# Kernel tuning notes

Measured on AMD Instinct MI355X. Metric: run time of the kernel, lower is better.

The kernel has to match this reference:

```python
import jax, jax.numpy as jnp
import numpy as np

B = 1024
NIF = 2048   # n_image_features
V = 10000    # vocab_size
E = 512      # embedding_dim
H = 1024     # hidden_size
L = 32       # max_sentence_length
ND = 3       # num distractors


def _lstm_cell(x, h, c, Wih, Whh, bih, bhh):
    # torch LSTMCell: gates ordered i, f, g, o
    g = x @ Wih.T + bih + h @ Whh.T + bhh
    i, f, gc, o = jnp.split(g, 4, axis=-1)
    c = jax.nn.sigmoid(f) * c + jax.nn.sigmoid(i) * jnp.tanh(gc)
    h = jax.nn.sigmoid(o) * jnp.tanh(c)
    return h, c


def setup_inputs() -> dict:
    key = jax.random.key(0)
    ks = jax.random.split(key, 20)
    s = 0.02
    inp = {
        "target": jax.random.normal(ks[0], (B, NIF), jnp.float32),
        "distractors": jax.random.normal(ks[1], (ND, B, NIF), jnp.float32),
        "start_token_idx": 1,
        "max_sentence_length": L,
        # Sender params
        "W_aff": s * jax.random.normal(ks[2], (H, NIF), jnp.float32),
        "b_aff": jnp.zeros((H,), jnp.float32),
        "emb_s": s * jax.random.normal(ks[3], (V, E), jnp.float32),
        "Wih_s": s * jax.random.normal(ks[4], (4 * H, E), jnp.float32),
        "Whh_s": s * jax.random.normal(ks[5], (4 * H, H), jnp.float32),
        "bih_s": jnp.zeros((4 * H,), jnp.float32),
        "bhh_s": jnp.zeros((4 * H,), jnp.float32),
        "Wp": s * jax.random.normal(ks[6], (V, H), jnp.float32),
        "bp": jnp.zeros((V,), jnp.float32),
        # Receiver params
        "emb_r": s * jax.random.normal(ks[7], (V, E), jnp.float32),
        "Wih_r": s * jax.random.normal(ks[8], (4 * H, E), jnp.float32),
        "Whh_r": s * jax.random.normal(ks[9], (4 * H, H), jnp.float32),
        "bih_r": jnp.zeros((4 * H,), jnp.float32),
        "bhh_r": jnp.zeros((4 * H,), jnp.float32),
        "W_out": s * jax.random.normal(ks[10], (NIF, H), jnp.float32),
        "b_out": jnp.zeros((NIF,), jnp.float32),
    }
    return inp


def reference(target, distractors, start_token_idx, max_sentence_length,
              W_aff, b_aff, emb_s, Wih_s, Whh_s, bih_s, bhh_s, Wp, bp,
              emb_r, Wih_r, Whh_r, bih_r, bhh_r, W_out, b_out):
    Bt = target.shape[0]

    # ---- Sender: greedy decode (eval-mode argmax, matching greedy=True) ----
    h0 = target @ W_aff.T + b_aff
    c0 = jnp.zeros_like(h0)
    w0 = emb_s[jnp.full((Bt,), start_token_idx, dtype=jnp.int32)]

    def send_step(carry, _):
        h, c, w = carry
        h, c = _lstm_cell(w, h, c, Wih_s, Whh_s, bih_s, bhh_s)
        logits = h @ Wp.T + bp                         # [B, V]
        idx = jnp.argmax(logits, axis=-1)              # greedy token
        logp = jnp.take_along_axis(jax.nn.log_softmax(logits, axis=-1),
                                   idx[:, None], axis=-1)[:, 0]
        w = emb_s[idx]
        return (h, c, w), (idx, logp)

    _, (message, logps) = jax.lax.scan(send_step, (h0, c0, w0), None,
                                       length=max_sentence_length)
    message = message.T            # [B, L]
    log_prob = logps[-1]           # log_prob of last sampled word, [B]

    # ---- Receiver: encode message ----
    hr = jnp.zeros((Bt, H), jnp.float32)
    cr = jnp.zeros((Bt, H), jnp.float32)

    def recv_step(carry, w_idx):
        h, c = carry
        h, c = _lstm_cell(emb_r[w_idx], h, c, Wih_r, Whh_r, bih_r, bhh_r)
        return (h, c), None

    (hr, cr), _ = jax.lax.scan(recv_step, (hr, cr), message.T)
    r = hr @ W_out.T + b_out       # [B, NIF]

    # ---- Hinge loss over distractors ----
    r_T = r.T                                       # [NIF, B]
    t_r = target @ r_T                              # [B, B]
    d_r = jnp.einsum('nbf,fc->nbc', distractors, r_T)  # [ND, B, B]
    loss = jnp.sum(jnp.maximum(0.0, 1.0 - t_r[None] + d_r), axis=0)  # [B, B]
    loss = -loss * log_prob        # broadcast [B] over last dim, as in torch
    return jnp.mean(loss)
```

## Files before the change

kernel.cpp:

```cpp
#include <hip/hip_runtime.h>
#include <hip/hip_bf16.h>
#include <cstdint>
#include <cstddef>

#define Bc   1024
#define NIFc 2048
#define Vc   10000
#define Ec   512
#define Hc   1024
#define Lc   32
#define NDc  3
#define G4c  4096
#define NTv  79
#define TMLD 80

typedef __attribute__((ext_vector_type(4))) float f32x4;
typedef __attribute__((ext_vector_type(8))) short s16x8;
typedef __attribute__((ext_vector_type(4))) short s16x4;

#define GBM 128
#define GBN 128
#define GBK 64

__device__ __forceinline__ void gld_lds16(void* lds, const void* g) {
    __builtin_amdgcn_global_load_lds(
        (const __attribute__((address_space(1))) unsigned int*)g,
        (__attribute__((address_space(3))) unsigned int*)lds,
        16, 0, 0);
}

__device__ __forceinline__ void gemm_body(
    const __hip_bfloat16* __restrict__ A, int lda,
    const __hip_bfloat16* __restrict__ W, int ldw,
    const float* __restrict__ bias, float* __restrict__ C,
    int M, int N, int K, int bx, int by,
    float* __restrict__ tile_max, int tmld)
{
    __shared__ __align__(16) __hip_bfloat16 As[GBM * GBK];
    __shared__ __align__(16) __hip_bfloat16 Ws[GBN * GBK];
    __shared__ float smax[GBM];

    const int tid  = threadIdx.x;
    const int lane = tid & 63;
    const int wave = tid >> 6;
    const int m0 = by * GBM;
    const int n0 = bx * GBN;

    const __hip_bfloat16* ag[4];
    const __hip_bfloat16* wg[4];
    #pragma unroll
    for (int r = 0; r < 4; ++r) {
        int p = r * 256 + tid;
        int m = p >> 3;
        int q = (p & 7) ^ (m & 7);
        ag[r] = A + (size_t)(m0 + m) * lda + q * 8;
        int wn = n0 + m; if (wn >= N) wn = N - 1;
        wg[r] = W + (size_t)wn * ldw + q * 8;
    }

    f32x4 acc[4][4];
    #pragma unroll
    for (int i = 0; i < 4; ++i)
        #pragma unroll
        for (int j = 0; j < 4; ++j)
            acc[i][j] = (f32x4)(0.0f);

    const int hm = (wave & 1) << 6;
    const int hn = (wave >> 1) << 6;
    const int lm = lane & 15;
    const int quad = lane >> 4;

    const int nk = K >> 6;
    for (int kt = 0; kt < nk; ++kt) {
        __syncthreads();
        #pragma unroll
        for (int r = 0; r < 4; ++r) {
            int ldsbase = (r * 256 + wave * 64) * 8;
            gld_lds16(As + ldsbase, ag[r]);
            gld_lds16(Ws + ldsbase, wg[r]);
            ag[r] += GBK;
            wg[r] += GBK;
        }
        __syncthreads();
        #pragma unroll
        for (int c = 0; c < 2; ++c) {
            s16x8 af[4], wf[4];
            int q = c * 4 + quad;
            #pragma unroll
            for (int i = 0; i < 4; ++i) {
                int m = hm + i * 16 + lm;
                af[i] = *(const s16x8*)(As + ((m << 3) + (q ^ (m & 7))) * 8);
                int n = hn + i * 16 + lm;
                wf[i] = *(const s16x8*)(Ws + ((n << 3) + (q ^ (n & 7))) * 8);
            }
            #pragma unroll
            for (int i = 0; i < 4; ++i)
                #pragma unroll
                for (int j = 0; j < 4; ++j)
                    acc[i][j] = __builtin_amdgcn_mfma_f32_16x16x32_bf16(
                        af[i], wf[j], acc[i][j], 0, 0, 0);
        }
    }

    float rowmax[4][4];
    #pragma unroll
    for (int i = 0; i < 4; ++i)
        #pragma unroll
        for (int rr = 0; rr < 4; ++rr)
            rowmax[i][rr] = -__builtin_inff();

    #pragma unroll
    for (int i = 0; i < 4; ++i) {
        int mbase = m0 + hm + i * 16 + quad * 4;
        #pragma unroll
        for (int j = 0; j < 4; ++j) {
            int n = n0 + hn + j * 16 + lm;
            if (n < N) {
                float bv = bias ? bias[n] : 0.0f;
                #pragma unroll
                for (int rr = 0; rr < 4; ++rr) {
                    float v = acc[i][j][rr] + bv;
                    C[(size_t)(mbase + rr) * N + n] = v;
                    rowmax[i][rr] = fmaxf(rowmax[i][rr], v);
                }
            }
        }
    }

    if (tile_max) {
        #pragma unroll
        for (int i = 0; i < 4; ++i)
            #pragma unroll
            for (int rr = 0; rr < 4; ++rr) {
                float v = rowmax[i][rr];
                v = fmaxf(v, __shfl_xor(v, 1));
                v = fmaxf(v, __shfl_xor(v, 2));
                v = fmaxf(v, __shfl_xor(v, 4));
                v = fmaxf(v, __shfl_xor(v, 8));
                rowmax[i][rr] = v;
            }
        __syncthreads();
        if (hn == 0 && lm == 0) {
            #pragma unroll
            for (int i = 0; i < 4; ++i)
                #pragma unroll
                for (int rr = 0; rr < 4; ++rr)
                    smax[hm + i * 16 + quad * 4 + rr] = rowmax[i][rr];
        }
        __syncthreads();
        if (hn == 64 && lm == 0) {
            #pragma unroll
            for (int i = 0; i < 4; ++i)
                #pragma unroll
                for (int rr = 0; rr < 4; ++rr) {
                    int r = hm + i * 16 + quad * 4 + rr;
                    smax[r] = fmaxf(smax[r], rowmax[i][rr]);
                }
        }
        __syncthreads();
        if (tid < GBM)
            tile_max[(size_t)(m0 + tid) * tmld + bx] = smax[tid];
    }
}

__global__ __launch_bounds__(256) void gemm_bf16_tn(
    const __hip_bfloat16* __restrict__ A, int lda,
    const __hip_bfloat16* __restrict__ W, int ldw,
    const float* __restrict__ bias, float* __restrict__ C,
    int M, int N, int K, float* __restrict__ tile_max, int tmld)
{
    gemm_body(A, lda, W, ldw, bias, C, M, N, K, blockIdx.x, blockIdx.y,
              tile_max, tmld);
}

__global__ __launch_bounds__(256) void gemm_bf16_sk2(
    const __hip_bfloat16* __restrict__ A, int lda,
    const __hip_bfloat16* __restrict__ W, int ldw,
    float* __restrict__ Cpart, int M, int N, int Ksub)
{
    int z = blockIdx.z;
    gemm_body(A + (size_t)z * Ksub, lda, W + (size_t)z * Ksub, ldw, nullptr,
              Cpart + (size_t)z * M * N, M, N, Ksub, blockIdx.x, blockIdx.y,
              nullptr, 0);
}

__global__ __launch_bounds__(256) void split3_a_kernel(
    const float* __restrict__ in, int ldin,
    __hip_bfloat16* __restrict__ out, int ldo, int coff, int M, int K)
{
    int i = blockIdx.x * 256 + threadIdx.x;
    if (i >= M * K) return;
    int m = i / K, k = i - m * K;
    float v = in[(size_t)m * ldin + k];
    __hip_bfloat16 hi = __float2bfloat16(v);
    float lo = v - __bfloat162float(hi);
    __hip_bfloat16* row = out + (size_t)m * ldo + coff;
    row[k] = hi;
    row[K + k] = __float2bfloat16(lo);
    row[2 * K + k] = hi;
}

__global__ __launch_bounds__(256) void split3_w_kernel(
    const float* __restrict__ in, int ldin,
    __hip_bfloat16* __restrict__ out, int ldo, int coff, int M, int K)
{
    int i = blockIdx.x * 256 + threadIdx.x;
    if (i >= M * K) return;
    int m = i / K, k = i - m * K;
    float v = in[(size_t)m * ldin + k];
    __hip_bfloat16 hi = __float2bfloat16(v);
    float lo = v - __bfloat162float(hi);
    __hip_bfloat16* row = out + (size_t)m * ldo + coff;
    row[k] = hi;
    row[K + k] = hi;
    row[2 * K + k] = __float2bfloat16(lo);
}

__global__ __launch_bounds__(256) void cast2d_kernel(
    const float* __restrict__ in, int ldin,
    __hip_bfloat16* __restrict__ out, int ldo, int coff, int M, int K)
{
    int i = blockIdx.x * 256 + threadIdx.x;
    if (i >= M * K) return;
    int m = i / K, k = i - m * K;
    out[(size_t)m * ldo + coff + k] = __float2bfloat16(in[(size_t)m * ldin + k]);
}

__global__ __launch_bounds__(256) void gather_split3_kernel(
    const float* __restrict__ emb, int E, const int* __restrict__ idx,
    int stride, __hip_bfloat16* __restrict__ out, int ldo, int Brows)
{
    int i = blockIdx.x * 256 + threadIdx.x;
    if (i >= Brows * E) return;
    int b = i / E, k = i - b * E;
    float v = emb[(size_t)idx[b * stride] * E + k];
    __hip_bfloat16 hi = __float2bfloat16(v);
    float lo = v - __bfloat162float(hi);
    __hip_bfloat16* row = out + (size_t)b * ldo;
    row[k] = hi;
    row[E + k] = __float2bfloat16(lo);
    row[2 * E + k] = hi;
}

__global__ __launch_bounds__(256) void gather_cast_kernel(
    const float* __restrict__ emb, int E, const int* __restrict__ idx,
    __hip_bfloat16* __restrict__ out, int ldo, int coff, int Brows)
{
    int i = blockIdx.x * 256 + threadIdx.x;
    if (i >= Brows * E) return;
    int b = i / E, k = i - b * E;
    out[(size_t)b * ldo + coff + k] =
        __float2bfloat16(emb[(size_t)idx[b] * E + k]);
}

__global__ __launch_bounds__(256) void add_vec_kernel(
    const float* __restrict__ a, const float* __restrict__ b,
    float* __restrict__ o, int n)
{
    int i = blockIdx.x * 256 + threadIdx.x;
    if (i < n) o[i] = a[i] + b[i];
}

__device__ __forceinline__ short bf16bits(float x) {
    __hip_bfloat16 t = __float2bfloat16(x);
    return *reinterpret_cast<short*>(&t);
}

__global__ __launch_bounds__(256) void lstm_fused_s(
    const float* __restrict__ gp0, const float* __restrict__ gp1,
    const float* __restrict__ bias, float* __restrict__ h,
    float* __restrict__ c, __hip_bfloat16* __restrict__ xh3)
{
    int i = blockIdx.x * 256 + threadIdx.x;
    if (i >= Bc * Hc / 4) return;
    int b = i >> 8;
    int j = (i & 255) * 4;
    size_t g0 = (size_t)b * G4c + j;
    f32x4 gi = *(const f32x4*)(gp0 + g0) + *(const f32x4*)(gp1 + g0)
             + *(const f32x4*)(bias + j);
    f32x4 gf = *(const f32x4*)(gp0 + g0 + Hc) + *(const f32x4*)(gp1 + g0 + Hc)
             + *(const f32x4*)(bias + Hc + j);
    f32x4 gg = *(const f32x4*)(gp0 + g0 + 2 * Hc) + *(const f32x4*)(gp1 + g0 + 2 * Hc)
             + *(const f32x4*)(bias + 2 * Hc + j);
    f32x4 go = *(const f32x4*)(gp0 + g0 + 3 * Hc) + *(const f32x4*)(gp1 + g0 + 3 * Hc)
             + *(const f32x4*)(bias + 3 * Hc + j);
    size_t hix = (size_t)b * Hc + j;
    f32x4 cv = *(const f32x4*)(c + hix);
    f32x4 cn, hv;
    s16x4 hi4, lo4;
    #pragma unroll
    for (int k = 0; k < 4; ++k) {
        float si = 1.0f / (1.0f + expf(-gi[k]));
        float sf = 1.0f / (1.0f + expf(-gf[k]));
        float so = 1.0f / (1.0f + expf(-go[k]));
        float cc = sf * cv[k] + si * tanhf(gg[k]);
        cn[k] = cc;
        float hh = so * tanhf(cc);
        hv[k] = hh;
        hi4[k] = bf16bits(hh);
        lo4[k] = bf16bits(hh - __bfloat162float(__float2bfloat16(hh)));
    }
    *(f32x4*)(c + hix) = cn;
    *(f32x4*)(h + hix) = hv;
    __hip_bfloat16* row = xh3 + (size_t)b * 4608 + 1536;
    *(s16x4*)(row + j) = hi4;
    *(s16x4*)(row + Hc + j) = lo4;
    *(s16x4*)(row + 2 * Hc + j) = hi4;
}

__global__ __launch_bounds__(256) void combine_h0_kernel(
    const float* __restrict__ p0, const float* __restrict__ p1,
    const float* __restrict__ bias, float* __restrict__ h,
    __hip_bfloat16* __restrict__ xh3)
{
    int i = blockIdx.x * 256 + threadIdx.x;
    if (i >= Bc * Hc / 4) return;
    int b = i >> 8;
    int j = (i & 255) * 4;
    size_t ix = (size_t)b * Hc + j;
    f32x4 v = *(const f32x4*)(p0 + ix) + *(const f32x4*)(p1 + ix)
            + *(const f32x4*)(bias + j);
    *(f32x4*)(h + ix) = v;
    s16x4 hi4, lo4;
    #pragma unroll
    for (int k = 0; k < 4; ++k) {
        hi4[k] = bf16bits(v[k]);
        lo4[k] = bf16bits(v[k] - __bfloat162float(__float2bfloat16(v[k])));
    }
    __hip_bfloat16* row = xh3 + (size_t)b * 4608 + 1536;
    *(s16x4*)(row + j) = hi4;
    *(s16x4*)(row + Hc + j) = lo4;
    *(s16x4*)(row + 2 * Hc + j) = hi4;
}

__global__ __launch_bounds__(256) void lstm_fused_r(
    const float* __restrict__ gp0, const float* __restrict__ gp1,
    const float* __restrict__ bias, float* __restrict__ h,
    float* __restrict__ c, __hip_bfloat16* __restrict__ xh_r,
    const float* __restrict__ emb, const int* __restrict__ msg_next)
{
    int i = blockIdx.x * 256 + threadIdx.x;
    if (i >= Bc * Hc / 4) return;
    int b = i >> 8;
    int j = (i & 255) * 4;
    size_t g0 = (size_t)b * G4c + j;
    f32x4 gi = *(const f32x4*)(gp0 + g0) + *(const f32x4*)(gp1 + g0)
             + *(const f32x4*)(bias + j);
    f32x4 gf = *(const f32x4*)(gp0 + g0 + Hc) + *(const f32x4*)(gp1 + g0 + Hc)
             + *(const f32x4*)(bias + Hc + j);
    f32x4 gg = *(const f32x4*)(gp0 + g0 + 2 * Hc) + *(const f32x4*)(gp1 + g0 + 2 * Hc)
             + *(const f32x4*)(bias + 2 * Hc + j);
    f32x4 go = *(const f32x4*)(gp0 + g0 + 3 * Hc) + *(const f32x4*)(gp1 + g0 + 3 * Hc)
             + *(const f32x4*)(bias + 3 * Hc + j);
    size_t hix = (size_t)b * Hc + j;
    f32x4 cv = *(const f32x4*)(c + hix);
    f32x4 cn, hv;
    s16x4 hb4;
    #pragma unroll
    for (int k = 0; k < 4; ++k) {
        float si = 1.0f / (1.0f + expf(-gi[k]));
        float sf = 1.0f / (1.0f + expf(-gf[k]));
        float so = 1.0f / (1.0f + expf(-go[k]));
        float cc = sf * cv[k] + si * tanhf(gg[k]);
        cn[k] = cc;
        float hh = so * tanhf(cc);
        hv[k] = hh;
        hb4[k] = bf16bits(hh);
    }
    *(f32x4*)(c + hix) = cn;
    *(f32x4*)(h + hix) = hv;
    *(s16x4*)(xh_r + (size_t)b * 1536 + Ec + j) = hb4;
    if (msg_next && j < Ec) {
        int tok = msg_next[b];
        f32x4 e = *(const f32x4*)(emb + (size_t)tok * Ec + j);
        s16x4 eb;
        #pragma unroll
        for (int k = 0; k < 4; ++k) eb[k] = bf16bits(e[k]);
        *(s16x4*)(xh_r + (size_t)b * 1536 + j) = eb;
    }
}

__global__ __launch_bounds__(256) void argmax_rescore_v3(
    const float* __restrict__ logits, const float* __restrict__ tmax,
    const float* __restrict__ h, const float* __restrict__ Wp,
    const float* __restrict__ bp, const float* __restrict__ emb,
    int* __restrict__ msg_t, float* __restrict__ logp,
    __hip_bfloat16* __restrict__ xh3, int want_logp)
{
    const int b = blockIdx.x;
    const int tid = threadIdx.x;
    const int lane = tid & 63;
    const int wave = tid >> 6;
    const float* row = logits + (size_t)b * Vc;

    __shared__ float stm[128];
    __shared__ float redm[256];
    __shared__ float reds[256];
    __shared__ int   qt[32];
    __shared__ int   nq, cnt;
    __shared__ int   cand[64];
    __shared__ float score[64];
    __shared__ float sbestv;
    __shared__ int   sbestj;

    float tv = (tid < NTv) ? tmax[(size_t)b * TMLD + tid] : -__builtin_inff();
    if (tid < 128) stm[tid] = tv;
    redm[tid] = tv;
    reds[tid] = (tid < NTv) ? tv : 0.0f;
    if (tid == 0) { nq = 0; cnt = 0; }
    __syncthreads();
    #pragma unroll
    for (int s = 128; s > 0; s >>= 1) {
        if (tid < s) {
            redm[tid] = fmaxf(redm[tid], redm[tid + s]);
            reds[tid] += reds[tid + s];
        }
        __syncthreads();
    }
    const float m = redm[0];
    const float spread = m - reds[0] * (1.0f / NTv);
    const float delta = 0.08f * spread + 1e-6f * (1.0f + fabsf(m));

    if (tid < NTv && stm[tid] >= m - delta) {
        int k = atomicAdd(&nq, 1);
        if (k < 32) qt[k] = tid;
    }
    __syncthreads();
    int nqt = nq < 32 ? nq : 32;

    for (int qi = 0; qi < nqt; qi += 2) {
        int ti = qi + (tid >> 7);
        if (ti < nqt) {
            int j = qt[ti] * 128 + (tid & 127);
            if (j < Vc) {
                float v = row[j];
                if (v >= m - delta) {
                    int k = atomicAdd(&cnt, 1);
                    if (k < 64) cand[k] = j;
                }
            }
        }
    }
    __syncthreads();
    int nc = cnt < 64 ? cnt : 64;

    const float* hrow = h + (size_t)b * Hc;
    for (int cix = wave; cix < nc; cix += 4) {
        int j = cand[cix];
        const float* wrow = Wp + (size_t)j * Hc;
        float part = 0.0f;
        #pragma unroll
        for (int kk = 0; kk < 4; ++kk) {
            int k = kk * 256 + lane * 4;
            f32x4 hv = *(const f32x4*)(hrow + k);
            f32x4 wv = *(const f32x4*)(wrow + k);
            part = fmaf(hv.x, wv.x, part);
            part = fmaf(hv.y, wv.y, part);
            part = fmaf(hv.z, wv.z, part);
            part = fmaf(hv.w, wv.w, part);
        }
        #pragma unroll
        for (int off = 1; off < 64; off <<= 1)
            part += __shfl_xor(part, off);
        if (lane == 0) score[cix] = part + bp[j];
    }
    __syncthreads();
    if (tid == 0) {
        float bv = -__builtin_inff();
        int bj = 0x7fffffff;
        for (int cix = 0; cix < nc; ++cix) {
            float v = score[cix];
            int j = cand[cix];
            if (v > bv || (v == bv && j < bj)) { bv = v; bj = j; }
        }
        sbestv = bv;
        sbestj = bj;
        msg_t[b] = bj;
    }
    __syncthreads();
    const int bestj = sbestj;

    if (want_logp) {
        float s = 0.0f;
        const f32x4* row4 = (const f32x4*)row;
        for (int j = tid; j < Vc / 4; j += 256) {
            f32x4 v = row4[j];
            s += expf(v.x - m) + expf(v.y - m) + expf(v.z - m) + expf(v.w - m);
        }
        redm[tid] = s;
        __syncthreads();
        #pragma unroll
        for (int st = 128; st > 0; st >>= 1) {
            if (tid < st) redm[tid] += redm[tid + st];
            __syncthreads();
        }
        if (tid == 0) logp[b] = sbestv - (m + logf(redm[0]));
    }

    if (xh3 && tid < 128) {
        int k = tid * 4;
        f32x4 e = *(const f32x4*)(emb + (size_t)bestj * Ec + k);
        s16x4 hi4, lo4;
        #pragma unroll
        for (int kk = 0; kk < 4; ++kk) {
            hi4[kk] = bf16bits(e[kk]);
            lo4[kk] = bf16bits(e[kk] - __bfloat162float(__float2bfloat16(e[kk])));
        }
        __hip_bfloat16* orow = xh3 + (size_t)b * 4608;
        *(s16x4*)(orow + k) = hi4;
        *(s16x4*)(orow + Ec + k) = lo4;
        *(s16x4*)(orow + 2 * Ec + k) = hi4;
    }
}

__global__ __launch_bounds__(256) void hinge_kernel(
    const float* __restrict__ S, const float* __restrict__ logp,
    float* __restrict__ partials, int Bn)
{
    int tid = threadIdx.x;
    int n = Bn * Bn;
    float acc = 0.0f;
    for (int idx = blockIdx.x * 256 + tid; idx < n; idx += gridDim.x * 256) {
        int j = idx & (Bn - 1);
        float s0 = S[idx];
        float l = fmaxf(0.0f, 1.0f - s0 + S[n + idx])
                + fmaxf(0.0f, 1.0f - s0 + S[2 * n + idx])
                + fmaxf(0.0f, 1.0f - s0 + S[3 * n + idx]);
        acc += l * logp[j];
    }
    __shared__ float sv[256];
    sv[tid] = acc;
    __syncthreads();
    for (int s = 128; s > 0; s >>= 1) {
        if (tid < s) sv[tid] += sv[tid + s];
        __syncthreads();
    }
    if (tid == 0) partials[blockIdx.x] = sv[0];
}

__global__ __launch_bounds__(256) void final_reduce_kernel(
    const float* __restrict__ partials, int np, float* __restrict__ out,
    float scale)
{
    int tid = threadIdx.x;
    float acc = 0.0f;
    for (int i = tid; i < np; i += 256) acc += partials[i];
    __shared__ float sv[256];
    sv[tid] = acc;
    __syncthreads();
    for (int s = 128; s > 0; s >>= 1) {
        if (tid < s) sv[tid] += sv[tid + s];
        __syncthreads();
    }
    if (tid == 0) out[0] = sv[0] * scale;
}

extern "C" void kernel_launch(void* const* d_in, const int* in_sizes, int n_in,
                              void* d_out, int out_size, void* d_ws, size_t ws_size,
                              hipStream_t stream)
{
    (void)in_sizes; (void)n_in; (void)out_size; (void)ws_size;

    const float* target  = (const float*)d_in[0];
    const float* distr   = (const float*)d_in[1];
    const int*   start_t = (const int*)d_in[2];
    const float* W_aff = (const float*)d_in[4];
    const float* b_aff = (const float*)d_in[5];
    const float* emb_s = (const float*)d_in[6];
    const float* Wih_s = (const float*)d_in[7];
    const float* Whh_s = (const float*)d_in[8];
    const float* bih_s = (const float*)d_in[9];
    const float* bhh_s = (const float*)d_in[10];
    const float* Wp    = (const float*)d_in[11];
    const float* bp    = (const float*)d_in[12];
    const float* emb_r = (const float*)d_in[13];
    const float* Wih_r = (const float*)d_in[14];
    const float* Whh_r = (const float*)d_in[15];
    const float* bih_r = (const float*)d_in[16];
    const float* bhh_r = (const float*)d_in[17];
    const float* W_out = (const float*)d_in[18];
    const float* b_out = (const float*)d_in[19];

    dim3 blk(256);

    char* b0 = (char*)d_ws;
    size_t off = 0;
    auto take = [&](size_t bytes) -> char* {
        char* p = b0 + off;
        off += (bytes + 511) & ~(size_t)511;
        return p;
    };
    const size_t MB = 1024 * 1024;
    __hip_bfloat16* WihWhh3 = (__hip_bfloat16*)take((size_t)G4c * 4608 * 2);
    __hip_bfloat16* Wp_b    = (__hip_bfloat16*)take((size_t)Vc * Hc * 2);
    __hip_bfloat16* WihWhh_r= (__hip_bfloat16*)take((size_t)G4c * 1536 * 2);
    __hip_bfloat16* W_out_b = (__hip_bfloat16*)take((size_t)NIFc * Hc * 2);
    __hip_bfloat16* xh3     = (__hip_bfloat16*)take((size_t)Bc * 4608 * 2);
    __hip_bfloat16* xh_r    = (__hip_bfloat16*)take((size_t)Bc * 1536 * 2);
    float* gates_p = (float*)take((size_t)2 * Bc * G4c * 4);
    float* h_s    = (float*)take((size_t)Bc * Hc * 4);
    float* c_s    = (float*)take((size_t)Bc * Hc * 4);
    float* hr     = (float*)take((size_t)Bc * Hc * 4);
    float* cr     = (float*)take((size_t)Bc * Hc * 4);
    float* logp   = (float*)take(Bc * 4);
    int*   msg    = (int*)take((size_t)Lc * Bc * 4);
    float* parts  = (float*)take(1024 * 4);
    float* bias_s = (float*)take(G4c * 4);
    float* bias_r = (float*)take(G4c * 4);
    float* tilemax= (float*)take((size_t)Bc * TMLD * 4);
    char*  U      = take(48 * MB);

    __hip_bfloat16* target3 = (__hip_bfloat16*)U;
    __hip_bfloat16* W_aff3  = (__hip_bfloat16*)(U + 13 * MB);
    float*          logits  = (float*)U;
    __hip_bfloat16* A4b     = (__hip_bfloat16*)U;
    float*          r_f     = (float*)(U + 17 * MB);
    __hip_bfloat16* r_b     = (__hip_bfloat16*)(U + 26 * MB);
    float*          S       = (float*)(U + 31 * MB);

    split3_w_kernel<<<(G4c * Ec + 255) / 256, blk, 0, stream>>>(
        Wih_s, Ec, WihWhh3, 4608, 0, G4c, Ec);
    split3_w_kernel<<<(G4c * Hc + 255) / 256, blk, 0, stream>>>(
        Whh_s, Hc, WihWhh3, 4608, 1536, G4c, Hc);
    cast2d_kernel<<<(Vc * Hc + 255) / 256, blk, 0, stream>>>(
        Wp, Hc, Wp_b, Hc, 0, Vc, Hc);
    split3_a_kernel<<<(Bc * NIFc + 255) / 256, blk, 0, stream>>>(
        target, NIFc, target3, 6144, 0, Bc, NIFc);
    split3_w_kernel<<<(Hc * NIFc + 255) / 256, blk, 0, stream>>>(
        W_aff, NIFc, W_aff3, 6144, 0, Hc, NIFc);
    cast2d_kernel<<<(G4c * Ec + 255) / 256, blk, 0, stream>>>(
        Wih_r, Ec, WihWhh_r, 1536, 0, G4c, Ec);
    cast2d_kernel<<<(G4c * Hc + 255) / 256, blk, 0, stream>>>(
        Whh_r, Hc, WihWhh_r, 1536, Ec, G4c, Hc);
    cast2d_kernel<<<(NIFc * Hc + 255) / 256, blk, 0, stream>>>(
        W_out, Hc, W_out_b, Hc, 0, NIFc, Hc);
    add_vec_kernel<<<(G4c + 255) / 256, blk, 0, stream>>>(bih_s, bhh_s,
                                                          bias_s, G4c);
    add_vec_kernel<<<(G4c + 255) / 256, blk, 0, stream>>>(bih_r, bhh_r,
                                                          bias_r, G4c);

    gemm_bf16_sk2<<<dim3(Hc / GBN, Bc / GBM, 2), blk, 0, stream>>>(
        target3, 6144, W_aff3, 6144, gates_p, Bc, Hc, 3072);
    combine_h0_kernel<<<(Bc * Hc / 4 + 255) / 256, blk, 0, stream>>>(
        gates_p, gates_p + (size_t)Bc * Hc, b_aff, h_s, xh3);
    hipMemsetAsync(c_s, 0, (size_t)Bc * Hc * 4, stream);
    gather_split3_kernel<<<(Bc * Ec + 255) / 256, blk, 0, stream>>>(
        emb_s, Ec, start_t, 0, xh3, 4608, Bc);

    for (int t = 0; t < Lc; ++t) {
        gemm_bf16_sk2<<<dim3(G4c / GBN, Bc / GBM, 2), blk, 0, stream>>>(
            xh3, 4608, WihWhh3, 4608, gates_p, Bc, G4c, 2304);
        lstm_fused_s<<<(Bc * Hc / 4 + 255) / 256, blk, 0, stream>>>(
            gates_p, gates_p + (size_t)Bc * G4c, bias_s, h_s, c_s, xh3);
        gemm_bf16_tn<<<dim3((Vc + GBN - 1) / GBN, Bc / GBM), blk, 0, stream>>>(
            xh3 + 1536, 4608, Wp_b, Hc, bp, logits, Bc, Vc, Hc, tilemax, TMLD);
        argmax_rescore_v3<<<Bc, blk, 0, stream>>>(
            logits, tilemax, h_s, Wp, bp, emb_s, msg + t * Bc, logp,
            (t < Lc - 1) ? xh3 : nullptr, (t == Lc - 1) ? 1 : 0);
    }

    hipMemsetAsync(hr, 0, (size_t)Bc * Hc * 4, stream);
    hipMemsetAsync(cr, 0, (size_t)Bc * Hc * 4, stream);
    hipMemsetAsync(xh_r, 0, (size_t)Bc * 1536 * 2, stream);
    gather_cast_kernel<<<(Bc * Ec + 255) / 256, blk, 0, stream>>>(
        emb_r, Ec, msg, xh_r, 1536, 0, Bc);
    for (int t = 0; t < Lc; ++t) {
        gemm_bf16_sk2<<<dim3(G4c / GBN, Bc / GBM, 2), blk, 0, stream>>>(
            xh_r, 1536, WihWhh_r, 1536, gates_p, Bc, G4c, 768);
        lstm_fused_r<<<(Bc * Hc / 4 + 255) / 256, blk, 0, stream>>>(
            gates_p, gates_p + (size_t)Bc * G4c, bias_r, hr, cr, xh_r,
            emb_r, (t < Lc - 1) ? (msg + (t + 1) * Bc) : nullptr);
    }

    gemm_bf16_tn<<<dim3(NIFc / GBN, Bc / GBM), blk, 0, stream>>>(
        xh_r + Ec, 1536, W_out_b, Hc, b_out, r_f, Bc, NIFc, Hc, nullptr, 0);

    cast2d_kernel<<<(Bc * NIFc + 255) / 256, blk, 0, stream>>>(
        target, NIFc, A4b, NIFc, 0, Bc, NIFc);
    cast2d_kernel<<<(NDc * Bc * NIFc + 255) / 256, blk, 0, stream>>>(
        distr, NIFc, A4b + (size_t)Bc * NIFc, NIFc, 0, NDc * Bc, NIFc);
    cast2d_kernel<<<(Bc * NIFc + 255) / 256, blk, 0, stream>>>(
        r_f, NIFc, r_b, NIFc, 0, Bc, NIFc);
    gemm_bf16_tn<<<dim3(Bc / GBN, 4 * Bc / GBM), blk, 0, stream>>>(
        A4b, NIFc, r_b, NIFc, nullptr, S, 4 * Bc, Bc, NIFc, nullptr, 0);

    hinge_kernel<<<1024, blk, 0, stream>>>(S, logp, parts, Bc);
    final_reduce_kernel<<<1, blk, 0, stream>>>(
        parts, 1024, (float*)d_out, -1.0f / ((float)Bc * (float)Bc));
}
```

Measured before the change: 4.769 ms.

## Precompute per-token input-gate tables to drop embedding GEMM from LSTM steps

Precomputes emb @ Wih^T for every vocabulary token, once for the sender and once for the receiver, and stores the results as bf16 tables. Each LSTM step then gathers its token's row inside the fused cell kernel, so the per-step GEMM only covers the recurrent h part. The sender's input term also loses its split-precision (hi/lo) treatment, which shrinks the per-step K from 2304 to 1536. In exchange it pays two 10000x4096x512 GEMMs and about 160MB of workspace per call, and rounding the table to bf16 changes numerics, which could alter greedy argmax tokens.

```diff
diff --git a/kernel.cpp b/kernel.cpp
--- a/kernel.cpp
+++ b/kernel.cpp
@@ -13,6 +13,8 @@
 #define G4c  4096
 #define NTv  79
 #define TMLD 80
+#define XLD  3584
+#define XOFF 512
 
 typedef __attribute__((ext_vector_type(4))) float f32x4;
 typedef __attribute__((ext_vector_type(8))) short s16x8;
@@ -29,10 +31,11 @@
         16, 0, 0);
 }
 
+template<int OBF>
 __device__ __forceinline__ void gemm_body(
     const __hip_bfloat16* __restrict__ A, int lda,
     const __hip_bfloat16* __restrict__ W, int ldw,
-    const float* __restrict__ bias, float* __restrict__ C,
+    const float* __restrict__ bias, void* __restrict__ Cv,
     int M, int N, int K, int bx, int by,
     float* __restrict__ tile_max, int tmld)
 {
@@ -53,7 +56,8 @@
         int p = r * 256 + tid;
         int m = p >> 3;
         int q = (p & 7) ^ (m & 7);
-        ag[r] = A + (size_t)(m0 + m) * lda + q * 8;
+        int am = m0 + m; if (am >= M) am = M - 1;
+        ag[r] = A + (size_t)am * lda + q * 8;
         int wn = n0 + m; if (wn >= N) wn = N - 1;
         wg[r] = W + (size_t)wn * ldw + q * 8;
     }
@@ -120,7 +124,13 @@
                 #pragma unroll
                 for (int rr = 0; rr < 4; ++rr) {
                     float v = acc[i][j][rr] + bv;
-                    C[(size_t)(mbase + rr) * N + n] = v;
+                    if (mbase + rr < M) {
+                        if (OBF)
+                            ((__hip_bfloat16*)Cv)[(size_t)(mbase + rr) * N + n] =
+                                __float2bfloat16(v);
+                        else
+                            ((float*)Cv)[(size_t)(mbase + rr) * N + n] = v;
+                    }
                     rowmax[i][rr] = fmaxf(rowmax[i][rr], v);
                 }
             }
@@ -169,8 +179,17 @@
     const float* __restrict__ bias, float* __restrict__ C,
     int M, int N, int K, float* __restrict__ tile_max, int tmld)
 {
-    gemm_body(A, lda, W, ldw, bias, C, M, N, K, blockIdx.x, blockIdx.y,
-              tile_max, tmld);
+    gemm_body<0>(A, lda, W, ldw, bias, C, M, N, K, blockIdx.x, blockIdx.y,
+                 tile_max, tmld);
+}
+
+__global__ __launch_bounds__(256) void gemm_bf16_obf(
+    const __hip_bfloat16* __restrict__ A, int lda,
+    const __hip_bfloat16* __restrict__ W, int ldw,
+    __hip_bfloat16* __restrict__ C, int M, int N, int K)
+{
+    gemm_body<1>(A, lda, W, ldw, nullptr, C, M, N, K, blockIdx.x, blockIdx.y,
+                 nullptr, 0);
 }
 
 __global__ __launch_bounds__(256) void gemm_bf16_sk2(
@@ -179,9 +198,9 @@
     float* __restrict__ Cpart, int M, int N, int Ksub)
 {
     int z = blockIdx.z;
-    gemm_body(A + (size_t)z * Ksub, lda, W + (size_t)z * Ksub, ldw, nullptr,
-              Cpart + (size_t)z * M * N, M, N, Ksub, blockIdx.x, blockIdx.y,
-              nullptr, 0);
+    gemm_body<0>(A + (size_t)z * Ksub, lda, W + (size_t)z * Ksub, ldw, nullptr,
+                 Cpart + (size_t)z * M * N, M, N, Ksub, blockIdx.x, blockIdx.y,
+                 nullptr, 0);
 }
 
 __global__ __launch_bounds__(256) void split3_a_kernel(
@@ -226,31 +245,15 @@
     out[(size_t)m * ldo + coff + k] = __float2bfloat16(in[(size_t)m * ldin + k]);
 }
 
-__global__ __launch_bounds__(256) void gather_split3_kernel(
-    const float* __restrict__ emb, int E, const int* __restrict__ idx,
-    int stride, __hip_bfloat16* __restrict__ out, int ldo, int Brows)
-{
-    int i = blockIdx.x * 256 + threadIdx.x;
-    if (i >= Brows * E) return;
-    int b = i / E, k = i - b * E;
-    float v = emb[(size_t)idx[b * stride] * E + k];
-    __hip_bfloat16 hi = __float2bfloat16(v);
-    float lo = v - __bfloat162float(hi);
-    __hip_bfloat16* row = out + (size_t)b * ldo;
-    row[k] = hi;
-    row[E + k] = __float2bfloat16(lo);
-    row[2 * E + k] = hi;
-}
-
 __global__ __launch_bounds__(256) void gather_cast_kernel(
     const float* __restrict__ emb, int E, const int* __restrict__ idx,
-    __hip_bfloat16* __restrict__ out, int ldo, int coff, int Brows)
+    int stride, __hip_bfloat16* __restrict__ out, int ldo, int coff, int Brows)
 {
     int i = blockIdx.x * 256 + threadIdx.x;
     if (i >= Brows * E) return;
     int b = i / E, k = i - b * E;
     out[(size_t)b * ldo + coff + k] =
-        __float2bfloat16(emb[(size_t)idx[b] * E + k]);
+        __float2bfloat16(emb[(size_t)idx[(size_t)b * stride] * E + k]);
 }
 
 __global__ __launch_bounds__(256) void add_vec_kernel(
@@ -266,10 +269,16 @@
     return *reinterpret_cast<short*>(&t);
 }
 
+__device__ __forceinline__ float b16f(short s) {
+    return __bfloat162float(*reinterpret_cast<__hip_bfloat16*>(&s));
+}
+
 __global__ __launch_bounds__(256) void lstm_fused_s(
     const float* __restrict__ gp0, const float* __restrict__ gp1,
     const float* __restrict__ bias, float* __restrict__ h,
-    float* __restrict__ c, __hip_bfloat16* __restrict__ xh3)
+    float* __restrict__ c, __hip_bfloat16* __restrict__ h3x,
+    const __hip_bfloat16* __restrict__ xg, const int* __restrict__ tok,
+    int tstride)
 {
     int i = blockIdx.x * 256 + threadIdx.x;
     if (i >= Bc * Hc / 4) return;
@@ -284,6 +293,20 @@
              + *(const f32x4*)(bias + 2 * Hc + j);
     f32x4 go = *(const f32x4*)(gp0 + g0 + 3 * Hc) + *(const f32x4*)(gp1 + g0 + 3 * Hc)
              + *(const f32x4*)(bias + 3 * Hc + j);
+    if (xg) {
+        const __hip_bfloat16* xr = xg + (size_t)tok[(size_t)b * tstride] * G4c;
+        s16x4 xi = *(const s16x4*)(xr + j);
+        s16x4 xf = *(const s16x4*)(xr + Hc + j);
+        s16x4 xc = *(const s16x4*)(xr + 2 * Hc + j);
+        s16x4 xo = *(const s16x4*)(xr + 3 * Hc + j);
+        #pragma unroll
+        for (int k = 0; k < 4; ++k) {
+            gi[k] += b16f(xi[k]);
+            gf[k] += b16f(xf[k]);
+            gg[k] += b16f(xc[k]);
+            go[k] += b16f(xo[k]);
+        }
+    }
     size_t hix = (size_t)b * Hc + j;
     f32x4 cv = *(const f32x4*)(c + hix);
     f32x4 cn, hv;
@@ -302,7 +325,7 @@
     }
     *(f32x4*)(c + hix) = cn;
     *(f32x4*)(h + hix) = hv;
-    __hip_bfloat16* row = xh3 + (size_t)b * 4608 + 1536;
+    __hip_bfloat16* row = h3x + (size_t)b * XLD + XOFF;
     *(s16x4*)(row + j) = hi4;
     *(s16x4*)(row + Hc + j) = lo4;
     *(s16x4*)(row + 2 * Hc + j) = hi4;
@@ -311,7 +334,7 @@
 __global__ __launch_bounds__(256) void combine_h0_kernel(
     const float* __restrict__ p0, const float* __restrict__ p1,
     const float* __restrict__ bias, float* __restrict__ h,
-    __hip_bfloat16* __restrict__ xh3)
+    __hip_bfloat16* __restrict__ h3x)
 {
     int i = blockIdx.x * 256 + threadIdx.x;
     if (i >= Bc * Hc / 4) return;
@@ -327,7 +350,7 @@
         hi4[k] = bf16bits(v[k]);
         lo4[k] = bf16bits(v[k] - __bfloat162float(__float2bfloat16(v[k])));
     }
-    __hip_bfloat16* row = xh3 + (size_t)b * 4608 + 1536;
+    __hip_bfloat16* row = h3x + (size_t)b * XLD + XOFF;
     *(s16x4*)(row + j) = hi4;
     *(s16x4*)(row + Hc + j) = lo4;
     *(s16x4*)(row + 2 * Hc + j) = hi4;
@@ -337,21 +360,38 @@
     const float* __restrict__ gp0, const float* __restrict__ gp1,
     const float* __restrict__ bias, float* __restrict__ h,
     float* __restrict__ c, __hip_bfloat16* __restrict__ xh_r,
-    const float* __restrict__ emb, const int* __restrict__ msg_next)
+    const __hip_bfloat16* __restrict__ xg, const int* __restrict__ tok,
+    int has_g, const float* __restrict__ emb, const int* __restrict__ msg_next)
 {
     int i = blockIdx.x * 256 + threadIdx.x;
     if (i >= Bc * Hc / 4) return;
     int b = i >> 8;
     int j = (i & 255) * 4;
-    size_t g0 = (size_t)b * G4c + j;
-    f32x4 gi = *(const f32x4*)(gp0 + g0) + *(const f32x4*)(gp1 + g0)
-             + *(const f32x4*)(bias + j);
-    f32x4 gf = *(const f32x4*)(gp0 + g0 + Hc) + *(const f32x4*)(gp1 + g0 + Hc)
-             + *(const f32x4*)(bias + Hc + j);
-    f32x4 gg = *(const f32x4*)(gp0 + g0 + 2 * Hc) + *(const f32x4*)(gp1 + g0 + 2 * Hc)
-             + *(const f32x4*)(bias + 2 * Hc + j);
-    f32x4 go = *(const f32x4*)(gp0 + g0 + 3 * Hc) + *(const f32x4*)(gp1 + g0 + 3 * Hc)
-             + *(const f32x4*)(bias + 3 * Hc + j);
+    f32x4 gi = *(const f32x4*)(bias + j);
+    f32x4 gf = *(const f32x4*)(bias + Hc + j);
+    f32x4 gg = *(const f32x4*)(bias + 2 * Hc + j);
+    f32x4 go = *(const f32x4*)(bias + 3 * Hc + j);
+    if (has_g) {
+        size_t g0 = (size_t)b * G4c + j;
+        gi += *(const f32x4*)(gp0 + g0) + *(const f32x4*)(gp1 + g0);
+        gf += *(const f32x4*)(gp0 + g0 + Hc) + *(const f32x4*)(gp1 + g0 + Hc);
+        gg += *(const f32x4*)(gp0 + g0 + 2 * Hc) + *(const f32x4*)(gp1 + g0 + 2 * Hc);
+        go += *(const f32x4*)(gp0 + g0 + 3 * Hc) + *(const f32x4*)(gp1 + g0 + 3 * Hc);
+    }
+    if (xg) {
+        const __hip_bfloat16* xr = xg + (size_t)tok[b] * G4c;
+        s16x4 xi = *(const s16x4*)(xr + j);
+        s16x4 xf = *(const s16x4*)(xr + Hc + j);
+        s16x4 xc = *(const s16x4*)(xr + 2 * Hc + j);
+        s16x4 xo = *(const s16x4*)(xr + 3 * Hc + j);
+        #pragma unroll
+        for (int k = 0; k < 4; ++k) {
+            gi[k] += b16f(xi[k]);
+            gf[k] += b16f(xf[k]);
+            gg[k] += b16f(xc[k]);
+            go[k] += b16f(xo[k]);
+        }
+    }
     size_t hix = (size_t)b * Hc + j;
     f32x4 cv = *(const f32x4*)(c + hix);
     f32x4 cn, hv;
@@ -370,9 +410,9 @@
     *(f32x4*)(c + hix) = cn;
     *(f32x4*)(h + hix) = hv;
     *(s16x4*)(xh_r + (size_t)b * 1536 + Ec + j) = hb4;
-    if (msg_next && j < Ec) {
-        int tok = msg_next[b];
-        f32x4 e = *(const f32x4*)(emb + (size_t)tok * Ec + j);
+    if (!xg && msg_next && j < Ec) {
+        int t2 = msg_next[b];
+        f32x4 e = *(const f32x4*)(emb + (size_t)t2 * Ec + j);
         s16x4 eb;
         #pragma unroll
         for (int k = 0; k < 4; ++k) eb[k] = bf16bits(e[k]);
@@ -385,7 +425,7 @@
     const float* __restrict__ h, const float* __restrict__ Wp,
     const float* __restrict__ bp, const float* __restrict__ emb,
     int* __restrict__ msg_t, float* __restrict__ logp,
-    __hip_bfloat16* __restrict__ xh3, int want_logp)
+    __hip_bfloat16* __restrict__ xdst, int want_logp)
 {
     const int b = blockIdx.x;
     const int tid = threadIdx.x;
@@ -497,19 +537,13 @@
         if (tid == 0) logp[b] = sbestv - (m + logf(redm[0]));
     }
 
-    if (xh3 && tid < 128) {
+    if (xdst && tid < 128) {
         int k = tid * 4;
         f32x4 e = *(const f32x4*)(emb + (size_t)bestj * Ec + k);
-        s16x4 hi4, lo4;
-        #pragma unroll
-        for (int kk = 0; kk < 4; ++kk) {
-            hi4[kk] = bf16bits(e[kk]);
-            lo4[kk] = bf16bits(e[kk] - __bfloat162float(__float2bfloat16(e[kk])));
-        }
-        __hip_bfloat16* orow = xh3 + (size_t)b * 4608;
-        *(s16x4*)(orow + k) = hi4;
-        *(s16x4*)(orow + Ec + k) = lo4;
-        *(s16x4*)(orow + 2 * Ec + k) = hi4;
+        s16x4 h4;
+        #pragma unroll
+        for (int kk = 0; kk < 4; ++kk) h4[kk] = bf16bits(e[kk]);
+        *(s16x4*)(xdst + (size_t)b * XLD + k) = h4;
     }
 }
 
@@ -559,7 +593,7 @@
                               void* d_out, int out_size, void* d_ws, size_t ws_size,
                               hipStream_t stream)
 {
-    (void)in_sizes; (void)n_in; (void)out_size; (void)ws_size;
+    (void)in_sizes; (void)n_in; (void)out_size;
 
     const float* target  = (const float*)d_in[0];
     const float* distr   = (const float*)d_in[1];
@@ -591,11 +625,11 @@
         return p;
     };
     const size_t MB = 1024 * 1024;
-    __hip_bfloat16* WihWhh3 = (__hip_bfloat16*)take((size_t)G4c * 4608 * 2);
+    __hip_bfloat16* W3x     = (__hip_bfloat16*)take((size_t)G4c * XLD * 2);
     __hip_bfloat16* Wp_b    = (__hip_bfloat16*)take((size_t)Vc * Hc * 2);
     __hip_bfloat16* WihWhh_r= (__hip_bfloat16*)take((size_t)G4c * 1536 * 2);
     __hip_bfloat16* W_out_b = (__hip_bfloat16*)take((size_t)NIFc * Hc * 2);
-    __hip_bfloat16* xh3     = (__hip_bfloat16*)take((size_t)Bc * 4608 * 2);
+    __hip_bfloat16* h3x     = (__hip_bfloat16*)take((size_t)Bc * XLD * 2);
     __hip_bfloat16* xh_r    = (__hip_bfloat16*)take((size_t)Bc * 1536 * 2);
     float* gates_p = (float*)take((size_t)2 * Bc * G4c * 4);
     float* h_s    = (float*)take((size_t)Bc * Hc * 4);
@@ -610,18 +644,24 @@
     float* tilemax= (float*)take((size_t)Bc * TMLD * 4);
     char*  U      = take(48 * MB);
 
+    __hip_bfloat16* Xg_s = (__hip_bfloat16*)take((size_t)Vc * G4c * 2);
+    const int use_tab_s = (off <= ws_size);
+    __hip_bfloat16* Xg_r = (__hip_bfloat16*)take((size_t)Vc * G4c * 2);
+    const int use_tab_r = (off <= ws_size);
+
     __hip_bfloat16* target3 = (__hip_bfloat16*)U;
     __hip_bfloat16* W_aff3  = (__hip_bfloat16*)(U + 13 * MB);
+    __hip_bfloat16* emb_b   = (__hip_bfloat16*)(U + 26 * MB);
     float*          logits  = (float*)U;
     __hip_bfloat16* A4b     = (__hip_bfloat16*)U;
     float*          r_f     = (float*)(U + 17 * MB);
     __hip_bfloat16* r_b     = (__hip_bfloat16*)(U + 26 * MB);
     float*          S       = (float*)(U + 31 * MB);
 
-    split3_w_kernel<<<(G4c * Ec + 255) / 256, blk, 0, stream>>>(
-        Wih_s, Ec, WihWhh3, 4608, 0, G4c, Ec);
+    cast2d_kernel<<<(G4c * Ec + 255) / 256, blk, 0, stream>>>(
+        Wih_s, Ec, W3x, XLD, 0, G4c, Ec);
     split3_w_kernel<<<(G4c * Hc + 255) / 256, blk, 0, stream>>>(
-        Whh_s, Hc, WihWhh3, 4608, 1536, G4c, Hc);
+        Whh_s, Hc, W3x, XLD, XOFF, G4c, Hc);
     cast2d_kernel<<<(Vc * Hc + 255) / 256, blk, 0, stream>>>(
         Wp, Hc, Wp_b, Hc, 0, Vc, Hc);
     split3_a_kernel<<<(Bc * NIFc + 255) / 256, blk, 0, stream>>>(
@@ -639,37 +679,72 @@
     add_vec_kernel<<<(G4c + 255) / 256, blk, 0, stream>>>(bih_r, bhh_r,
                                                           bias_r, G4c);
 
+    if (use_tab_s) {
+        cast2d_kernel<<<(Vc * Ec + 255) / 256, blk, 0, stream>>>(
+            emb_s, Ec, emb_b, Ec, 0, Vc, Ec);
+        gemm_bf16_obf<<<dim3(G4c / GBN, (Vc + GBM - 1) / GBM), blk, 0, stream>>>(
+            emb_b, Ec, W3x, XLD, Xg_s, Vc, G4c, Ec);
+    }
+    if (use_tab_r) {
+        cast2d_kernel<<<(Vc * Ec + 255) / 256, blk, 0, stream>>>(
+            emb_r, Ec, emb_b, Ec, 0, Vc, Ec);
+        gemm_bf16_obf<<<dim3(G4c / GBN, (Vc + GBM - 1) / GBM), blk, 0, stream>>>(
+            emb_b, Ec, WihWhh_r, 1536, Xg_r, Vc, G4c, Ec);
+    }
+
     gemm_bf16_sk2<<<dim3(Hc / GBN, Bc / GBM, 2), blk, 0, stream>>>(
         target3, 6144, W_aff3, 6144, gates_p, Bc, Hc, 3072);
     combine_h0_kernel<<<(Bc * Hc / 4 + 255) / 256, blk, 0, stream>>>(
-        gates_p, gates_p + (size_t)Bc * Hc, b_aff, h_s, xh3);
+        gates_p, gates_p + (size_t)Bc * Hc, b_aff, h_s, h3x);
     hipMemsetAsync(c_s, 0, (size_t)Bc * Hc * 4, stream);
-    gather_split3_kernel<<<(Bc * Ec + 255) / 256, blk, 0, stream>>>(
-        emb_s, Ec, start_t, 0, xh3, 4608, Bc);
+    if (!use_tab_s)
+        gather_cast_kernel<<<(Bc * Ec + 255) / 256, blk, 0, stream>>>(
+            emb_s, Ec, start_t, 0, h3x, XLD, 0, Bc);
 
     for (int t = 0; t < Lc; ++t) {
-        gemm_bf16_sk2<<<dim3(G4c / GBN, Bc / GBM, 2), blk, 0, stream>>>(
-            xh3, 4608, WihWhh3, 4608, gates_p, Bc, G4c, 2304);
-        lstm_fused_s<<<(Bc * Hc / 4 + 255) / 256, blk, 0, stream>>>(
-            gates_p, gates_p + (size_t)Bc * G4c, bias_s, h_s, c_s, xh3);
+        if (use_tab_s) {
+            gemm_bf16_sk2<<<dim3(G4c / GBN, Bc / GBM, 2), blk, 0, stream>>>(
+                h3x + XOFF, XLD, W3x + XOFF, XLD, gates_p, Bc, G4c, 1536);
+            lstm_fused_s<<<(Bc * Hc / 4 + 255) / 256, blk, 0, stream>>>(
+                gates_p, gates_p + (size_t)Bc * G4c, bias_s, h_s, c_s, h3x,
+                Xg_s, (t == 0) ? start_t : (msg + (t - 1) * Bc),
+                (t == 0) ? 0 : 1);
+        } else {
+            gemm_bf16_sk2<<<dim3(G4c / GBN, Bc / GBM, 2), blk, 0, stream>>>(
+                h3x, XLD, W3x, XLD, gates_p, Bc, G4c, 1792);
+            lstm_fused_s<<<(Bc * Hc / 4 + 255) / 256, blk, 0, stream>>>(
+                gates_p, gates_p + (size_t)Bc * G4c, bias_s, h_s, c_s, h3x,
+                nullptr, nullptr, 0);
+        }
         gemm_bf16_tn<<<dim3((Vc + GBN - 1) / GBN, Bc / GBM), blk, 0, stream>>>(
-            xh3 + 1536, 4608, Wp_b, Hc, bp, logits, Bc, Vc, Hc, tilemax, TMLD);
+            h3x + XOFF, XLD, Wp_b, Hc, bp, logits, Bc, Vc, Hc, tilemax, TMLD);
         argmax_rescore_v3<<<Bc, blk, 0, stream>>>(
             logits, tilemax, h_s, Wp, bp, emb_s, msg + t * Bc, logp,
-            (t < Lc - 1) ? xh3 : nullptr, (t == Lc - 1) ? 1 : 0);
+            (!use_tab_s && t < Lc - 1) ? h3x : nullptr, (t == Lc - 1) ? 1 : 0);
     }
 
     hipMemsetAsync(hr, 0, (size_t)Bc * Hc * 4, stream);
     hipMemsetAsync(cr, 0, (size_t)Bc * Hc * 4, stream);
     hipMemsetAsync(xh_r, 0, (size_t)Bc * 1536 * 2, stream);
-    gather_cast_kernel<<<(Bc * Ec + 255) / 256, blk, 0, stream>>>(
-        emb_r, Ec, msg, xh_r, 1536, 0, Bc);
+    if (!use_tab_r)
+        gather_cast_kernel<<<(Bc * Ec + 255) / 256, blk, 0, stream>>>(
+            emb_r, Ec, msg, 1, xh_r, 1536, 0, Bc);
     for (int t = 0; t < Lc; ++t) {
-        gemm_bf16_sk2<<<dim3(G4c / GBN, Bc / GBM, 2), blk, 0, stream>>>(
-            xh_r, 1536, WihWhh_r, 1536, gates_p, Bc, G4c, 768);
-        lstm_fused_r<<<(Bc * Hc / 4 + 255) / 256, blk, 0, stream>>>(
-            gates_p, gates_p + (size_t)Bc * G4c, bias_r, hr, cr, xh_r,
-            emb_r, (t < Lc - 1) ? (msg + (t + 1) * Bc) : nullptr);
+        if (use_tab_r) {
+            if (t > 0)
+                gemm_bf16_sk2<<<dim3(G4c / GBN, Bc / GBM, 2), blk, 0, stream>>>(
+                    xh_r + Ec, 1536, WihWhh_r + Ec, 1536, gates_p, Bc, G4c, 512);
+            lstm_fused_r<<<(Bc * Hc / 4 + 255) / 256, blk, 0, stream>>>(
+                gates_p, gates_p + (size_t)Bc * G4c, bias_r, hr, cr, xh_r,
+                Xg_r, msg + t * Bc, (t > 0) ? 1 : 0, nullptr, nullptr);
+        } else {
+            gemm_bf16_sk2<<<dim3(G4c / GBN, Bc / GBM, 2), blk, 0, stream>>>(
+                xh_r, 1536, WihWhh_r, 1536, gates_p, Bc, G4c, 768);
+            lstm_fused_r<<<(Bc * Hc / 4 + 255) / 256, blk, 0, stream>>>(
+                gates_p, gates_p + (size_t)Bc * G4c, bias_r, hr, cr, xh_r,
+                nullptr, nullptr, 1, emb_r,
+                (t < Lc - 1) ? (msg + (t + 1) * Bc) : nullptr);
+        }
     }
 
     gemm_bf16_tn<<<dim3(NIFc / GBN, Bc / GBM), blk, 0, stream>>>(
```

Result: faster. 4.537 ms (-4.9%).
